# Kernel optimization log

Measured on AMD Instinct MI355X. Metric: run time of the kernel, lower is better.

Reference implementation:

```python
import jax, jax.numpy as jnp
import numpy as np

NODES_PER_GRAPH = 21
N_GRAPHS = 50_000
N = N_GRAPHS * NODES_PER_GRAPH      # 1,050,000 nodes
E = 2_100_000                        # directed edges
NUM_CLASSES = 26


def setup_inputs() -> dict:
    key = jax.random.key(0)
    ks = jax.random.split(key, 8)
    x = jax.random.normal(ks[0], (N, 2), dtype=jnp.float32)
    src = jax.random.randint(ks[1], (E,), 0, N, dtype=jnp.int32)
    dst = jax.random.randint(ks[2], (E,), 0, N, dtype=jnp.int32)
    batch = (jnp.arange(N, dtype=jnp.int32) // NODES_PER_GRAPH)
    W1 = jax.random.normal(ks[3], (2, 64), dtype=jnp.float32) * 0.5
    b1 = jnp.zeros((64,), dtype=jnp.float32)
    W2 = jax.random.normal(ks[4], (64, 128), dtype=jnp.float32) * 0.125
    b2 = jnp.zeros((128,), dtype=jnp.float32)
    Wfc = jax.random.normal(ks[5], (128, 26), dtype=jnp.float32) * 0.088
    bfc = jnp.zeros((26,), dtype=jnp.float32)
    return {"x": x, "src": src, "dst": dst, "batch": batch,
            "W1": W1, "b1": b1, "W2": W2, "b2": b2, "Wfc": Wfc, "bfc": bfc}


def _gcn_conv(x, W, b, src_l, dst_l, norm, n_nodes):
    # PyG GCNConv: linear transform, then normalized scatter-add aggregation, then bias.
    xw = x @ W                                # [N, F_out]
    msg = xw[src_l] * norm[:, None]           # gather + scale per edge (incl. self-loops)
    out = jax.ops.segment_sum(msg, dst_l, num_segments=n_nodes)
    return out + b


def reference(x, src, dst, batch, W1, b1, W2, b2, Wfc, bfc):
    n = x.shape[0]
    loops = jnp.arange(n, dtype=src.dtype)
    # add self-loops (GCNConv default add_self_loops=True)
    src_l = jnp.concatenate([src, loops])
    dst_l = jnp.concatenate([dst, loops])
    # symmetric normalization: deg over target nodes, norm_e = d^-1/2[src] * d^-1/2[dst]
    deg = jax.ops.segment_sum(jnp.ones_like(dst_l, dtype=x.dtype), dst_l, num_segments=n)
    dinv = jnp.where(deg > 0, jax.lax.rsqrt(deg), 0.0)
    norm = dinv[src_l] * dinv[dst_l]

    h = jax.nn.relu(_gcn_conv(x, W1, b1, src_l, dst_l, norm, n))
    # F.dropout with training=False in eval mode -> identity
    h = _gcn_conv(h, W2, b2, src_l, dst_l, norm, n)

    # global_mean_pool over batch assignment
    n_graphs = N_GRAPHS
    sums = jax.ops.segment_sum(h, batch, num_segments=n_graphs)
    cnts = jax.ops.segment_sum(jnp.ones((n,), dtype=h.dtype), batch, num_segments=n_graphs)
    pooled = sums / jnp.maximum(cnts, 1.0)[:, None]   # [G, 128]

    logits = pooled @ Wfc + bfc
    return jax.nn.log_softmax(logits, axis=1)
```

## Files before the change

### kernel.cpp

```cpp
#include <hip/hip_runtime.h>
#include <hip/hip_fp16.h>
#include <math.h>

#define NODES   1050000
#define EDGES   2100000
#define GRAPHS  50000
#define NPG     21
#define NCLS    26
#define REC_MAX 168

#define NBUCK   1024
#define GPB     49
#define NPB     (GPB*NPG)
#define NPB_PAD 1088
#define BCAP    2816
#define NBLK_A  256
#define NTHR_A  1024
#define NTHR_H  1024
#define EPB     ((EDGES + NBLK_A - 1) / NBLK_A)
#define EITER   9
#define HITER   3

#define WAVE_FENCE() do { \
    asm volatile("s_waitcnt lgkmcnt(0)" ::: "memory"); \
    __builtin_amdgcn_sched_barrier(0); \
} while (0)

static __device__ __forceinline__ __half2 h2relu(__half2 h) {
    unsigned int u = *reinterpret_cast<unsigned int*>(&h);
    unsigned int r;
    asm("v_pk_max_f16 %0, %1, %2" : "=v"(r) : "v"(u), "v"(0u));
    return *reinterpret_cast<__half2*>(&r);
}

typedef _Float16 hf2 __attribute__((ext_vector_type(2)));
static __device__ __forceinline__ float fdot2(__half2 a, __half2 b, float c) {
#if __has_builtin(__builtin_amdgcn_fdot2)
    return __builtin_amdgcn_fdot2(*reinterpret_cast<hf2*>(&a),
                                  *reinterpret_cast<hf2*>(&b), c, false);
#else
    float2 fa = __half22float2(a), fb = __half22float2(b);
    return fmaf(fa.x, fb.x, fmaf(fa.y, fb.y, c));
#endif
}
static __device__ __forceinline__ float fdot2u(unsigned int a, unsigned int b, float c) {
    return fdot2(*reinterpret_cast<__half2*>(&a), *reinterpret_cast<__half2*>(&b), c);
}

__global__ void __launch_bounds__(NTHR_A) bucket_k(const int* __restrict__ src,
                                                   const int* __restrict__ dst,
                                                   int* __restrict__ bcnt,
                                                   unsigned int* __restrict__ arena) {
    __shared__ int hist[NBUCK];
    __shared__ int gbase[NBUCK];
    int tid = threadIdx.x;
    int rs[EITER], rd[EITER];
    for (int b = tid; b < NBUCK; b += NTHR_A) hist[b] = 0;
    __syncthreads();
    int e0 = blockIdx.x * EPB;
    int e1 = e0 + EPB; if (e1 > EDGES) e1 = EDGES;
    #pragma unroll
    for (int j = 0; j < EITER; ++j) {
        int e = e0 + tid + j * NTHR_A;
        if (e < e1) {
            int s = src[e], d = dst[e];
            rs[j] = s; rd[j] = d;
            atomicAdd(&hist[d / (NPG * GPB)], 1);
        }
    }
    __syncthreads();
    for (int b = tid; b < NBUCK; b += NTHR_A) {
        int h = hist[b];
        gbase[b] = h ? atomicAdd(&bcnt[b], h) : 0;
        hist[b] = 0;
    }
    __syncthreads();
    #pragma unroll
    for (int j = 0; j < EITER; ++j) {
        int e = e0 + tid + j * NTHR_A;
        if (e < e1) {
            int s = rs[j], d = rd[j];
            int g = d / NPG;
            int b = g / GPB;
            int r = atomicAdd(&hist[b], 1);
            int pos = gbase[b] + r;
            if (pos < BCAP)
                arena[(size_t)b * BCAP + pos] =
                    ((unsigned int)s << 11) | ((unsigned int)(g - b * GPB) << 5)
                    | (unsigned int)(d - g * NPG);
        }
    }
}

__global__ void __launch_bounds__(NTHR_H) histplace_k(const int* __restrict__ bcnt,
                                                      const unsigned int* __restrict__ arena,
                                                      const float* __restrict__ x,
                                                      int* __restrict__ ecnt,
                                                      int* __restrict__ eoff,
                                                      int* __restrict__ pe,
                                                      int* __restrict__ nfo,
                                                      unsigned int* __restrict__ up,
                                                      const float* __restrict__ W2,
                                                      const float* __restrict__ b2,
                                                      const float* __restrict__ Wfc,
                                                      const float* __restrict__ bfc,
                                                      float* __restrict__ wcomb,
                                                      float* __restrict__ bcomb,
                                                      unsigned int* __restrict__ wch) {
    int b = blockIdx.x, tid = threadIdx.x;
    if (b == NBUCK) {
        for (int t = tid; t < 64 * NCLS + NCLS; t += NTHR_H) {
            if (t < 64 * NCLS) {
                int f = t / NCLS, c = t % NCLS;
                float acc = 0.f;
                for (int k = 0; k < 128; ++k) acc += W2[f * 128 + k] * Wfc[k * NCLS + c];
                wcomb[t] = acc;
            } else {
                int c = t - 64 * NCLS;
                float acc = bfc[c];
                for (int k = 0; k < 128; ++k) acc += b2[k] * Wfc[k * NCLS + c];
                bcomb[c] = acc;
            }
        }
        __syncthreads();
        for (int t = tid; t < 32 * NCLS; t += NTHR_H) {
            int fp = t / NCLS, c = t % NCLS;
            const float s = 1.0f / (float)NPG;
            __half2 hh = __floats2half2_rn(wcomb[(2 * fp) * NCLS + c] * s,
                                           wcomb[(2 * fp + 1) * NCLS + c] * s);
            wch[t] = *reinterpret_cast<unsigned int*>(&hh);
        }
        return;
    }
    __shared__ int h[NPB];
    __shared__ int go2[NPB_PAD];
    __shared__ int wtot[17];
    __shared__ int gsum[GPB];
    unsigned int rc[HITER];
    int lane = tid & 63, wv = tid >> 6;
    for (int i = tid; i < NPB; i += NTHR_H) h[i] = 0;
    __syncthreads();
    int n = bcnt[b]; if (n > BCAP) n = BCAP;
    const unsigned int* ar = arena + (size_t)b * BCAP;
    #pragma unroll
    for (int j = 0; j < HITER; ++j) {
        int i = tid + j * NTHR_H;
        if (i < n) {
            unsigned int rec = ar[i];
            rc[j] = rec;
            atomicAdd(&h[((rec >> 5) & 63) * NPG + (rec & 31)], 1);
        }
    }
    __syncthreads();
    int nb0 = b * NPB;
    for (int i = tid; i < NPB; i += NTHR_H) {
        int node = nb0 + i;
        if (node < NODES) {
            float d = rsqrtf((float)(h[i] + 1));
            float2 xv = ((const float2*)x)[node];
            __half2 hh = __floats2half2_rn(d * xv.x, d * xv.y);
            up[node] = *reinterpret_cast<unsigned int*>(&hh);
        }
    }
    if (tid < GPB) {
        int s = 0;
        #pragma unroll
        for (int k = 0; k < NPG; ++k) s += h[tid * NPG + k];
        gsum[tid] = s;
    }
    for (int c = wv; c < 17; c += 16) {
        int idx = c * 64 + lane;
        int val = (idx < NPB) ? h[idx] : 0;
        int v = val;
        #pragma unroll
        for (int o = 1; o < 64; o <<= 1) { int t = __shfl_up(v, o, 64); if (lane >= o) v += t; }
        go2[idx] = v - val;
        if (lane == 63) wtot[c] = v;
    }
    __syncthreads();
    if (wv == 0) {
        int val = (lane < 17) ? wtot[lane] : 0;
        int v = val;
        #pragma unroll
        for (int o = 1; o < 32; o <<= 1) { int t = __shfl_up(v, o, 64); if (lane >= o) v += t; }
        if (lane < 17) wtot[lane] = v - val;
    }
    __syncthreads();
    for (int i = tid; i < NPB; i += NTHR_H) {
        int f = go2[i] + wtot[i >> 6];
        go2[i] = f;
        int node = nb0 + i;
        int deg = h[i] > 255 ? 255 : h[i];
        if (node < NODES) nfo[node] = (f << 8) | deg;
    }
    __syncthreads();
    if (wv == 0 && lane < GPB) {
        int g = b * GPB + lane;
        if (g < GRAPHS) { eoff[g] = b * BCAP + go2[lane * NPG]; ecnt[g] = gsum[lane]; }
    }
    __syncthreads();
    #pragma unroll
    for (int j = 0; j < HITER; ++j) {
        int i = tid + j * NTHR_H;
        if (i < n) {
            unsigned int rec = rc[j];
            int idx = ((rec >> 5) & 63) * NPG + (rec & 31);
            int pos = b * BCAP + atomicAdd(&go2[idx], 1);
            pe[pos] = (int)(((rec >> 11) << 5) | (rec & 31));
        }
    }
}

__global__ void __launch_bounds__(256) conv1_k(const int* __restrict__ nfo,
                                               const int* __restrict__ pe,
                                               const unsigned int* __restrict__ up,
                                               unsigned int* __restrict__ zh) {
    int i = blockIdx.x * 256 + threadIdx.x;
    if (i >= NODES) return;
    int b = i / NPB;
    int info = nfo[i];
    int off = b * BCAP + (info >> 8);
    int deg = info & 255;
    unsigned int raw = up[i];
    __half2 hs = *reinterpret_cast<__half2*>(&raw);
    float2 a = __half22float2(hs);
    int j = 0;
    for (; j + 2 <= deg; j += 2) {
        int p0 = pe[off + j], p1 = pe[off + j + 1];
        unsigned int r0 = up[p0 >> 5], r1 = up[p1 >> 5];
        __half2 h0 = *reinterpret_cast<__half2*>(&r0);
        __half2 h1 = *reinterpret_cast<__half2*>(&r1);
        float2 u0 = __half22float2(h0), u1 = __half22float2(h1);
        a.x += u0.x + u1.x;
        a.y += u0.y + u1.y;
    }
    if (j < deg) {
        int p0 = pe[off + j];
        unsigned int r0 = up[p0 >> 5];
        __half2 h0 = *reinterpret_cast<__half2*>(&r0);
        float2 u0 = __half22float2(h0);
        a.x += u0.x;
        a.y += u0.y;
    }
    int kk = deg + 1;
    float dv = rsqrtf((float)kk);
    if (kk > 63) kk = 63;
    __half2 h = __floats2half2_rn(dv * a.x, dv * a.y);
    unsigned int zb = *reinterpret_cast<unsigned int*>(&h);
    unsigned int lo = ((zb & 0xFFFFu) + 4u) & 0xFFF8u;
    unsigned int hi = (((zb >> 16) & 0xFFFFu) + 4u) & 0xFFF8u;
    zh[i] = (lo | (unsigned int)(kk & 7)) | ((hi | (unsigned int)(kk >> 3)) << 16);
}

#define RPL 3
__global__ void conv2pool_k(const int* __restrict__ pe, const int* __restrict__ eoff,
                            const int* __restrict__ ecnt,
                            const unsigned int* __restrict__ zh,
                            const float* __restrict__ W1, const float* __restrict__ b1,
                            const unsigned int* __restrict__ wch,
                            const float* __restrict__ bcomb,
                            float* __restrict__ out) {
    __shared__ unsigned short zxl[4][2][REC_MAX];
    __shared__ unsigned short zyl[4][2][REC_MAX];
    __shared__ unsigned short cfl[4][2][REC_MAX];
    __shared__ unsigned int ps2[4][32];
    __shared__ unsigned int lwch[32 * NCLS];
    int tid = threadIdx.x;
    int lane = tid & 63, wv = tid >> 6;
    for (int i = tid; i < 32 * NCLS; i += 256) lwch[i] = wch[i];
    __syncthreads();

    const __half2 w0h = __float2half2_rn(W1[lane]);
    const __half2 w1h = __float2half2_rn(W1[64 + lane]);
    const __half2 bbh = __float2half2_rn(b1[lane]);

    int gA = (blockIdx.x * 4 + wv) * 2;
    int gB = gA + 1;
    int baseA = gA * NPG, baseB = gB * NPG;
    int offA = eoff[gA], offB = eoff[gB];
    int cgA = ecnt[gA]; if (cgA > REC_MAX - NPG) cgA = REC_MAX - NPG;
    int cgB = ecnt[gB]; if (cgB > REC_MAX - NPG) cgB = REC_MAX - NPG;

    int pA[RPL], pB[RPL];
    unsigned int selfA = 0, selfB = 0;
    #pragma unroll
    for (int j = 0; j < RPL; ++j) {
        int iA = lane + j * 64;
        if (iA < cgA) pA[j] = __builtin_nontemporal_load(&pe[offA + iA]);
        int iB = lane + j * 64;
        if (iB < cgB) pB[j] = __builtin_nontemporal_load(&pe[offB + iB]);
    }
    if (lane < NPG) { selfA = zh[baseA + lane]; selfB = zh[baseB + lane]; }

    unsigned int rA[RPL], dA[RPL], rB[RPL], dB[RPL];
    #pragma unroll
    for (int j = 0; j < RPL; ++j) {
        if (lane + j * 64 < cgA) {
            rA[j] = zh[pA[j] >> 5];
            dA[j] = zh[baseA + (pA[j] & 31)];
        }
    }
    #pragma unroll
    for (int j = 0; j < RPL; ++j) {
        if (lane + j * 64 < cgB) {
            rB[j] = zh[pB[j] >> 5];
            dB[j] = zh[baseB + (pB[j] & 31)];
        }
    }

    int nrecA  = cgA + NPG;
    int nrec8A = (nrecA + 7) & ~7;
    #pragma unroll
    for (int j = 0; j < RPL; ++j) {
        int i = lane + j * 64;
        if (i < cgA) {
            unsigned int raw = rA[j], rd = dA[j];
            unsigned int kk = (raw & 7u) | (((raw >> 16) & 7u) << 3);
            unsigned int kd = (rd & 7u) | (((rd >> 16) & 7u) << 3);
            float cfv = rsqrtf((float)kk) * rsqrtf((float)kd);
            zxl[wv][0][i] = (unsigned short)(raw & 0xFFF8u);
            zyl[wv][0][i] = (unsigned short)((raw >> 16) & 0xFFF8u);
            __half cf = __float2half(cfv);
            cfl[wv][0][i] = *reinterpret_cast<unsigned short*>(&cf);
        }
    }
    if (lane < NPG) {
        unsigned int raw = selfA;
        unsigned int kk = (raw & 7u) | (((raw >> 16) & 7u) << 3);
        int i = cgA + lane;
        zxl[wv][0][i] = (unsigned short)(raw & 0xFFF8u);
        zyl[wv][0][i] = (unsigned short)((raw >> 16) & 0xFFF8u);
        __half cf = __float2half(1.0f / (float)kk);
        cfl[wv][0][i] = *reinterpret_cast<unsigned short*>(&cf);
    } else if (lane - NPG < nrec8A - nrecA) {
        int i = nrecA + (lane - NPG);
        zxl[wv][0][i] = 0; zyl[wv][0][i] = 0; cfl[wv][0][i] = 0;
    }
    WAVE_FENCE();

    #pragma unroll 1
    for (int half = 0; half < 2; ++half) {
        int hsel = half;
        const uint4* px = (const uint4*)zxl[wv][hsel];
        const uint4* py = (const uint4*)zyl[wv][hsel];
        const uint4* pc = (const uint4*)cfl[wv][hsel];
        int n8 = ((hsel ? nrec8A : nrec8A)) >> 3;
        (void)n8;
        break;
    }

    {
        const uint4* px = (const uint4*)zxl[wv][0];
        const uint4* py = (const uint4*)zyl[wv][0];
        const uint4* pc = (const uint4*)cfl[wv][0];
        float acc = 0.f;
        int n8 = nrec8A >> 3;
        for (int r = 0; r < n8; ++r) {
            uint4 X = px[r], Y = py[r], C = pc[r];
            {
                __half2 zx = *reinterpret_cast<__half2*>(&X.x);
                __half2 zy = *reinterpret_cast<__half2*>(&Y.x);
                __half2 cf = *reinterpret_cast<__half2*>(&C.x);
                acc = fdot2(h2relu(__hfma2(zx, w0h, __hfma2(zy, w1h, bbh))), cf, acc);
            }
            {
                __half2 zx = *reinterpret_cast<__half2*>(&X.y);
                __half2 zy = *reinterpret_cast<__half2*>(&Y.y);
                __half2 cf = *reinterpret_cast<__half2*>(&C.y);
                acc = fdot2(h2relu(__hfma2(zx, w0h, __hfma2(zy, w1h, bbh))), cf, acc);
            }
            {
                __half2 zx = *reinterpret_cast<__half2*>(&X.z);
                __half2 zy = *reinterpret_cast<__half2*>(&Y.z);
                __half2 cf = *reinterpret_cast<__half2*>(&C.z);
                acc = fdot2(h2relu(__hfma2(zx, w0h, __hfma2(zy, w1h, bbh))), cf, acc);
            }
            {
                __half2 zx = *reinterpret_cast<__half2*>(&X.w);
                __half2 zy = *reinterpret_cast<__half2*>(&Y.w);
                __half2 cf = *reinterpret_cast<__half2*>(&C.w);
                acc = fdot2(h2relu(__hfma2(zx, w0h, __hfma2(zy, w1h, bbh))), cf, acc);
            }
        }
        float s0 = __shfl(acc, 2 * (lane & 31), 64);
        float s1 = __shfl(acc, 2 * (lane & 31) + 1, 64);
        if (lane < 32) {
            __half2 hh = __floats2half2_rn(s0, s1);
            ps2[wv][lane] = *reinterpret_cast<unsigned int*>(&hh);
        }
        WAVE_FENCE();
        float part = 0.f;
        if (lane < 52) {
            int c  = (lane < NCLS) ? lane : lane - NCLS;
            int f0 = (lane < NCLS) ? 0 : 16;
            #pragma unroll
            for (int fp = 0; fp < 16; ++fp)
                part = fdot2u(ps2[wv][f0 + fp], lwch[(f0 + fp) * NCLS + c], part);
        }
        float other = __shfl(part, lane + NCLS, 64);
        float logit = 0.f;
        if (lane < NCLS) logit = bcomb[lane] + part + other;
        float m = (lane < NCLS) ? logit : -INFINITY;
        #pragma unroll
        for (int o = 16; o; o >>= 1) m = fmaxf(m, __shfl_xor(m, o, 32));
        float ex = (lane < NCLS) ? __expf(logit - m) : 0.f;
        float s = ex;
        #pragma unroll
        for (int o = 16; o; o >>= 1) s += __shfl_xor(s, o, 32);
        if (lane < NCLS) out[gA * NCLS + lane] = logit - m - __logf(s);
        WAVE_FENCE();
    }

    int nrecB  = cgB + NPG;
    int nrec8B = (nrecB + 7) & ~7;
    #pragma unroll
    for (int j = 0; j < RPL; ++j) {
        int i = lane + j * 64;
        if (i < cgB) {
            unsigned int raw = rB[j], rd = dB[j];
            unsigned int kk = (raw & 7u) | (((raw >> 16) & 7u) << 3);
            unsigned int kd = (rd & 7u) | (((rd >> 16) & 7u) << 3);
            float cfv = rsqrtf((float)kk) * rsqrtf((float)kd);
            zxl[wv][1][i] = (unsigned short)(raw & 0xFFF8u);
            zyl[wv][1][i] = (unsigned short)((raw >> 16) & 0xFFF8u);
            __half cf = __float2half(cfv);
            cfl[wv][1][i] = *reinterpret_cast<unsigned short*>(&cf);
        }
    }
    if (lane < NPG) {
        unsigned int raw = selfB;
        unsigned int kk = (raw & 7u) | (((raw >> 16) & 7u) << 3);
        int i = cgB + lane;
        zxl[wv][1][i] = (unsigned short)(raw & 0xFFF8u);
        zyl[wv][1][i] = (unsigned short)((raw >> 16) & 0xFFF8u);
        __half cf = __float2half(1.0f / (float)kk);
        cfl[wv][1][i] = *reinterpret_cast<unsigned short*>(&cf);
    } else if (lane - NPG < nrec8B - nrecB) {
        int i = nrecB + (lane - NPG);
        zxl[wv][1][i] = 0; zyl[wv][1][i] = 0; cfl[wv][1][i] = 0;
    }
    WAVE_FENCE();

    {
        const uint4* px = (const uint4*)zxl[wv][1];
        const uint4* py = (const uint4*)zyl[wv][1];
        const uint4* pc = (const uint4*)cfl[wv][1];
        float acc = 0.f;
        int n8 = nrec8B >> 3;
        for (int r = 0; r < n8; ++r) {
            uint4 X = px[r], Y = py[r], C = pc[r];
            {
                __half2 zx = *reinterpret_cast<__half2*>(&X.x);
                __half2 zy = *reinterpret_cast<__half2*>(&Y.x);
                __half2 cf = *reinterpret_cast<__half2*>(&C.x);
                acc = fdot2(h2relu(__hfma2(zx, w0h, __hfma2(zy, w1h, bbh))), cf, acc);
            }
            {
                __half2 zx = *reinterpret_cast<__half2*>(&X.y);
                __half2 zy = *reinterpret_cast<__half2*>(&Y.y);
                __half2 cf = *reinterpret_cast<__half2*>(&C.y);
                acc = fdot2(h2relu(__hfma2(zx, w0h, __hfma2(zy, w1h, bbh))), cf, acc);
            }
            {
                __half2 zx = *reinterpret_cast<__half2*>(&X.z);
                __half2 zy = *reinterpret_cast<__half2*>(&Y.z);
                __half2 cf = *reinterpret_cast<__half2*>(&C.z);
                acc = fdot2(h2relu(__hfma2(zx, w0h, __hfma2(zy, w1h, bbh))), cf, acc);
            }
            {
                __half2 zx = *reinterpret_cast<__half2*>(&X.w);
                __half2 zy = *reinterpret_cast<__half2*>(&Y.w);
                __half2 cf = *reinterpret_cast<__half2*>(&C.w);
                acc = fdot2(h2relu(__hfma2(zx, w0h, __hfma2(zy, w1h, bbh))), cf, acc);
            }
        }
        float s0 = __shfl(acc, 2 * (lane & 31), 64);
        float s1 = __shfl(acc, 2 * (lane & 31) + 1, 64);
        if (lane < 32) {
            __half2 hh = __floats2half2_rn(s0, s1);
            ps2[wv][lane] = *reinterpret_cast<unsigned int*>(&hh);
        }
        WAVE_FENCE();
        float part = 0.f;
        if (lane < 52) {
            int c  = (lane < NCLS) ? lane : lane - NCLS;
            int f0 = (lane < NCLS) ? 0 : 16;
            #pragma unroll
            for (int fp = 0; fp < 16; ++fp)
                part = fdot2u(ps2[wv][f0 + fp], lwch[(f0 + fp) * NCLS + c], part);
        }
        float other = __shfl(part, lane + NCLS, 64);
        float logit = 0.f;
        if (lane < NCLS) logit = bcomb[lane] + part + other;
        float m = (lane < NCLS) ? logit : -INFINITY;
        #pragma unroll
        for (int o = 16; o; o >>= 1) m = fmaxf(m, __shfl_xor(m, o, 32));
        float ex = (lane < NCLS) ? __expf(logit - m) : 0.f;
        float s = ex;
        #pragma unroll
        for (int o = 16; o; o >>= 1) s += __shfl_xor(s, o, 32);
        if (lane < NCLS) out[gB * NCLS + lane] = logit - m - __logf(s);
    }
}

extern "C" void kernel_launch(void* const* d_in, const int* in_sizes, int n_in,
                              void* d_out, int out_size, void* d_ws, size_t ws_size,
                              hipStream_t stream) {
    const float* x   = (const float*)d_in[0];
    const int*   src = (const int*)  d_in[1];
    const int*   dst = (const int*)  d_in[2];
    const float* W1  = (const float*)d_in[4];
    const float* b1  = (const float*)d_in[5];
    const float* W2  = (const float*)d_in[6];
    const float* b2  = (const float*)d_in[7];
    const float* Wfc = (const float*)d_in[8];
    const float* bfc = (const float*)d_in[9];
    float* out = (float*)d_out;

    char* ws = (char*)d_ws;
    size_t off = 0;
    auto carve = [&](size_t bytes) { char* p = ws + off; off += (bytes + 255) & ~(size_t)255; return p; };
    int*           ecnt  = (int*)           carve((size_t)GRAPHS * 4);
    int*           eoff  = (int*)           carve((size_t)GRAPHS * 4);
    int*           bcnt  = (int*)           carve((size_t)NBUCK * 4);
    unsigned int*  up    = (unsigned int*)  carve((size_t)NODES * 4);
    unsigned int*  zh    = (unsigned int*)  carve((size_t)NODES * 4);
    int*           nfo   = (int*)           carve((size_t)NODES * 4);
    int*           pe    = (int*)           carve((size_t)NBUCK * BCAP * 4);
    unsigned int*  arena = (unsigned int*)  carve((size_t)NBUCK * BCAP * 4);
    float*         wcomb = (float*)         carve((size_t)64 * NCLS * 4);
    float*         bcomb = (float*)         carve((size_t)NCLS * 4);
    unsigned int*  wch   = (unsigned int*)  carve((size_t)32 * NCLS * 4);
    (void)ws_size;

    hipMemsetAsync(bcnt, 0, (size_t)NBUCK * 4, stream);

    bucket_k   <<<NBLK_A, NTHR_A, 0, stream>>>(src, dst, bcnt, arena);
    histplace_k<<<NBUCK + 1, NTHR_H, 0, stream>>>(bcnt, arena, x, ecnt, eoff, pe, nfo,
                                                  up, W2, b2, Wfc, bfc,
                                                  wcomb, bcomb, wch);
    conv1_k    <<<(NODES + 255) / 256, 256, 0, stream>>>(nfo, pe, up, zh);
    conv2pool_k<<<GRAPHS / 8, 256, 0, stream>>>(pe, eoff, ecnt, zh, W1, b1,
                                                wch, bcomb, out);
}
```

Measured before the change: 119.5 us.

## Pack destination degree into edge records and double edge-pass block count

The bucketing kernel now stores the clamped destination degree in the top 6 bits of each packed edge record, so conv2pool no longer issues a second gather of zh for the destination node and computes the norm with one rsqrt of the product. Consumers mask the source index to 21 bits. Separately, the edge-scatter pass launches twice as many blocks with fewer iterations each, to raise parallelism. Dead loop code is removed. This assumes node indices fit in 21 bits and degrees are capped at 63.

```diff
diff --git a/kernel.cpp b/kernel.cpp
--- a/kernel.cpp
+++ b/kernel.cpp
@@ -14,11 +14,11 @@
 #define NPB     (GPB*NPG)
 #define NPB_PAD 1088
 #define BCAP    2816
-#define NBLK_A  256
+#define NBLK_A  512
 #define NTHR_A  1024
 #define NTHR_H  1024
 #define EPB     ((EDGES + NBLK_A - 1) / NBLK_A)
-#define EITER   9
+#define EITER   5
 #define HITER   3
 
 #define WAVE_FENCE() do { \
@@ -205,8 +205,10 @@
         if (i < n) {
             unsigned int rec = rc[j];
             int idx = ((rec >> 5) & 63) * NPG + (rec & 31);
+            int kd = h[idx] + 1; if (kd > 63) kd = 63;
             int pos = b * BCAP + atomicAdd(&go2[idx], 1);
-            pe[pos] = (int)(((rec >> 11) << 5) | (rec & 31));
+            pe[pos] = (int)(((rec >> 11) << 5) | (rec & 31)
+                            | ((unsigned int)kd << 26));
         }
     }
 }
@@ -226,8 +228,10 @@
     float2 a = __half22float2(hs);
     int j = 0;
     for (; j + 2 <= deg; j += 2) {
-        int p0 = pe[off + j], p1 = pe[off + j + 1];
-        unsigned int r0 = up[p0 >> 5], r1 = up[p1 >> 5];
+        unsigned int p0 = (unsigned int)pe[off + j];
+        unsigned int p1 = (unsigned int)pe[off + j + 1];
+        unsigned int r0 = up[(p0 >> 5) & 0x1FFFFFu];
+        unsigned int r1 = up[(p1 >> 5) & 0x1FFFFFu];
         __half2 h0 = *reinterpret_cast<__half2*>(&r0);
         __half2 h1 = *reinterpret_cast<__half2*>(&r1);
         float2 u0 = __half22float2(h0), u1 = __half22float2(h1);
@@ -235,8 +239,8 @@
         a.y += u0.y + u1.y;
     }
     if (j < deg) {
-        int p0 = pe[off + j];
-        unsigned int r0 = up[p0 >> 5];
+        unsigned int p0 = (unsigned int)pe[off + j];
+        unsigned int r0 = up[(p0 >> 5) & 0x1FFFFFu];
         __half2 h0 = *reinterpret_cast<__half2*>(&r0);
         float2 u0 = __half22float2(h0);
         a.x += u0.x;
@@ -281,32 +285,23 @@
     int cgA = ecnt[gA]; if (cgA > REC_MAX - NPG) cgA = REC_MAX - NPG;
     int cgB = ecnt[gB]; if (cgB > REC_MAX - NPG) cgB = REC_MAX - NPG;
 
-    int pA[RPL], pB[RPL];
+    unsigned int pA[RPL], pB[RPL];
     unsigned int selfA = 0, selfB = 0;
     #pragma unroll
     for (int j = 0; j < RPL; ++j) {
-        int iA = lane + j * 64;
-        if (iA < cgA) pA[j] = __builtin_nontemporal_load(&pe[offA + iA]);
-        int iB = lane + j * 64;
-        if (iB < cgB) pB[j] = __builtin_nontemporal_load(&pe[offB + iB]);
+        int i = lane + j * 64;
+        if (i < cgA) pA[j] = (unsigned int)__builtin_nontemporal_load(&pe[offA + i]);
+        if (i < cgB) pB[j] = (unsigned int)__builtin_nontemporal_load(&pe[offB + i]);
     }
     if (lane < NPG) { selfA = zh[baseA + lane]; selfB = zh[baseB + lane]; }
 
-    unsigned int rA[RPL], dA[RPL], rB[RPL], dB[RPL];
-    #pragma unroll
-    for (int j = 0; j < RPL; ++j) {
-        if (lane + j * 64 < cgA) {
-            rA[j] = zh[pA[j] >> 5];
-            dA[j] = zh[baseA + (pA[j] & 31)];
-        }
-    }
-    #pragma unroll
-    for (int j = 0; j < RPL; ++j) {
-        if (lane + j * 64 < cgB) {
-            rB[j] = zh[pB[j] >> 5];
-            dB[j] = zh[baseB + (pB[j] & 31)];
-        }
-    }
+    unsigned int rA[RPL], rB[RPL];
+    #pragma unroll
+    for (int j = 0; j < RPL; ++j)
+        if (lane + j * 64 < cgA) rA[j] = zh[(pA[j] >> 5) & 0x1FFFFFu];
+    #pragma unroll
+    for (int j = 0; j < RPL; ++j)
+        if (lane + j * 64 < cgB) rB[j] = zh[(pB[j] >> 5) & 0x1FFFFFu];
 
     int nrecA  = cgA + NPG;
     int nrec8A = (nrecA + 7) & ~7;
@@ -314,10 +309,10 @@
     for (int j = 0; j < RPL; ++j) {
         int i = lane + j * 64;
         if (i < cgA) {
-            unsigned int raw = rA[j], rd = dA[j];
+            unsigned int raw = rA[j];
             unsigned int kk = (raw & 7u) | (((raw >> 16) & 7u) << 3);
-            unsigned int kd = (rd & 7u) | (((rd >> 16) & 7u) << 3);
-            float cfv = rsqrtf((float)kk) * rsqrtf((float)kd);
+            unsigned int kd = pA[j] >> 26;
+            float cfv = rsqrtf((float)(kk * kd));
             zxl[wv][0][i] = (unsigned short)(raw & 0xFFF8u);
             zyl[wv][0][i] = (unsigned short)((raw >> 16) & 0xFFF8u);
             __half cf = __float2half(cfv);
@@ -338,17 +333,6 @@
     }
     WAVE_FENCE();
 
-    #pragma unroll 1
-    for (int half = 0; half < 2; ++half) {
-        int hsel = half;
-        const uint4* px = (const uint4*)zxl[wv][hsel];
-        const uint4* py = (const uint4*)zyl[wv][hsel];
-        const uint4* pc = (const uint4*)cfl[wv][hsel];
-        int n8 = ((hsel ? nrec8A : nrec8A)) >> 3;
-        (void)n8;
-        break;
-    }
-
     {
         const uint4* px = (const uint4*)zxl[wv][0];
         const uint4* py = (const uint4*)zyl[wv][0];
@@ -417,10 +401,10 @@
     for (int j = 0; j < RPL; ++j) {
         int i = lane + j * 64;
         if (i < cgB) {
-            unsigned int raw = rB[j], rd = dB[j];
+            unsigned int raw = rB[j];
             unsigned int kk = (raw & 7u) | (((raw >> 16) & 7u) << 3);
-            unsigned int kd = (rd & 7u) | (((rd >> 16) & 7u) << 3);
-            float cfv = rsqrtf((float)kk) * rsqrtf((float)kd);
+            unsigned int kd = pB[j] >> 26;
+            float cfv = rsqrtf((float)(kk * kd));
             zxl[wv][1][i] = (unsigned short)(raw & 0xFFF8u);
             zyl[wv][1][i] = (unsigned short)((raw >> 16) & 0xFFF8u);
             __half cf = __float2half(cfv);
```

Result: slower. 123.4 us (+3.2%).
